# Performance work log

Hardware: AMD Instinct MI355X
Metric: run time of the kernel (lower is better)

The kernel has to match this reference:

```python
import jax, jax.numpy as jnp
import numpy as np

N_M, N_H = 50000, 50000
E = 600000
D_IN, D_OUT = 128, 128
LN_EPS = 1e-5
NORM_EPS = 1e-12


def _segment_mean(x, seg, n):
    # PyG 'mean' aggregation: sum / count, 0 for isolated nodes (count clamped to 1)
    s = jax.ops.segment_sum(x, seg, num_segments=n)
    c = jax.ops.segment_sum(jnp.ones((seg.shape[0], 1), x.dtype), seg, num_segments=n)
    return s / jnp.maximum(c, 1.0)


def _sage(t_src, t_dst, ei, Wl, bl, Wr):
    # SAGEConv: lin_l(mean_j x_j) + lin_r(x_i), then L2-normalize rows
    agg = _segment_mean(t_src[ei[0]], ei[1], t_dst.shape[0])
    out = agg @ Wl + bl + t_dst @ Wr
    nrm = jnp.maximum(jnp.linalg.norm(out, axis=-1, keepdims=True), NORM_EPS)
    return out / nrm


def _layer_norm(x, g, b):
    mu = jnp.mean(x, axis=-1, keepdims=True)
    v = jnp.var(x, axis=-1, keepdims=True)
    return (x - mu) / jnp.sqrt(v + LN_EPS) * g + b


def setup_inputs() -> dict:
    key = jax.random.key(0)
    ks = jax.random.split(key, 24)
    r = lambda i, shape: jax.random.normal(ks[i], shape, dtype=jnp.float32) * 0.05
    inp = {
        'x_microbe': jax.random.normal(ks[0], (N_M, D_IN), dtype=jnp.float32),
        'x_host': jax.random.normal(ks[1], (N_H, D_IN), dtype=jnp.float32),
        # per-node-type linear transforms
        'W_nt_m': r(2, (D_IN, D_OUT)), 'b_nt_m': r(3, (D_OUT,)),
        'W_nt_h': r(4, (D_IN, D_OUT)), 'b_nt_h': r(5, (D_OUT,)),
        # SAGEConv params per edge type (lin_l has bias, lin_r has no bias)
        'Wl_mm': r(6, (D_OUT, D_OUT)), 'bl_mm': r(7, (D_OUT,)), 'Wr_mm': r(8, (D_OUT, D_OUT)),
        'Wl_mh': r(9, (D_OUT, D_OUT)), 'bl_mh': r(10, (D_OUT,)), 'Wr_mh': r(11, (D_OUT, D_OUT)),
        'Wl_hm': r(12, (D_OUT, D_OUT)), 'bl_hm': r(13, (D_OUT,)), 'Wr_hm': r(14, (D_OUT, D_OUT)),
        # LayerNorm affine params per node type
        'g_m': jnp.ones((D_OUT,), jnp.float32), 'be_m': jnp.zeros((D_OUT,), jnp.float32),
        'g_h': jnp.ones((D_OUT,), jnp.float32), 'be_h': jnp.zeros((D_OUT,), jnp.float32),
        # edge indices [2, E]: row0 = src, row1 = dst
        'ei_mm': jax.random.randint(ks[15], (2, E), 0, N_M, dtype=jnp.int32),
        'ei_mh': jnp.stack([jax.random.randint(ks[16], (E,), 0, N_M, dtype=jnp.int32),
                            jax.random.randint(ks[17], (E,), 0, N_H, dtype=jnp.int32)]),
        'ei_hm': jnp.stack([jax.random.randint(ks[18], (E,), 0, N_H, dtype=jnp.int32),
                            jax.random.randint(ks[19], (E,), 0, N_M, dtype=jnp.int32)]),
    }
    return inp


def reference(x_microbe, x_host, W_nt_m, b_nt_m, W_nt_h, b_nt_h,
              Wl_mm, bl_mm, Wr_mm, Wl_mh, bl_mh, Wr_mh, Wl_hm, bl_hm, Wr_hm,
              g_m, be_m, g_h, be_h, ei_mm, ei_mh, ei_hm):
    # per-type linear transforms
    t_m = x_microbe @ W_nt_m + b_nt_m
    t_h = x_host @ W_nt_h + b_nt_h
    # SAGEConv per edge type
    o_mm = _sage(t_m, t_m, ei_mm, Wl_mm, bl_mm, Wr_mm)  # microbe -> microbe
    o_mh = _sage(t_m, t_h, ei_mh, Wl_mh, bl_mh, Wr_mh)  # microbe -> host
    o_hm = _sage(t_h, t_m, ei_hm, Wl_hm, bl_hm, Wr_hm)  # host -> microbe
    # HeteroConv aggr='mean' over edge types per dst node type
    conv_m = 0.5 * (o_mm + o_hm)
    conv_h = o_mh
    # residual + LayerNorm (dropout is identity in eval mode)
    out_m = _layer_norm(t_m + conv_m, g_m, be_m)
    out_h = _layer_norm(t_h + conv_h, g_h, be_h)
    return out_m, out_h
```

## Files before the change

kernel.cpp:

```cpp
#include <hip/hip_runtime.h>

typedef unsigned short u16;
typedef unsigned int u32;
typedef __attribute__((ext_vector_type(8))) short bf16x8;
typedef __attribute__((ext_vector_type(4))) float f32x4;

#define LDSN 13312
#define CHUNK 131072

__device__ __forceinline__ float bf_lo(u32 u){ return __uint_as_float(u << 16); }
__device__ __forceinline__ float bf_hi(u32 u){ return __uint_as_float(u & 0xffff0000u); }
__device__ __forceinline__ float bf2f(u16 v){ return __uint_as_float((u32)v << 16); }
__device__ __forceinline__ u16 f2bf(float f){
    u32 u = __float_as_uint(f);
    u32 r = (u + 0x7fffu + ((u >> 16) & 1u)) >> 16;
    return (u16)r;
}
__device__ __forceinline__ u32 pack2(float a, float b){
    return (u32)f2bf(a) | ((u32)f2bf(b) << 16);
}

__global__ __launch_bounds__(256) void fusedA_kernel(
    const int* __restrict__ d0, const int* __restrict__ d1, const int* __restrict__ d2,
    u16* __restrict__ rk0, u16* __restrict__ rk1, u16* __restrict__ rk2,
    int E0, int E1, int E2, int n0, int n1, int n2,
    int c0, int c1, int c2, int R0, int R1, int R2,
    u16* __restrict__ C0, u16* __restrict__ C1, u16* __restrict__ C2, int HB2,
    const float* __restrict__ Wf0, const float* __restrict__ Wf1,
    const float* __restrict__ Wf2, const float* __restrict__ Wf3,
    const float* __restrict__ Wf4, const float* __restrict__ Wf5,
    u16* __restrict__ WF,
    const float* __restrict__ Xm, const float* __restrict__ Wm,
    const float* __restrict__ bm, u16* __restrict__ Tm, int NM,
    const float* __restrict__ Xh, const float* __restrict__ Wh,
    const float* __restrict__ bh, u16* __restrict__ Th, int NH,
    int gm, int gh)
{
    __shared__ u32 lc[LDSN / 2];
    int bid = blockIdx.x;
    if (bid < HB2){
        const int* dp; u16 *rk, *cp; int E, n, cc, rr;
        if (bid < c0 * R0){ dp = d0; rk = rk0; cp = C0; E = E0; n = n0; cc = bid / R0; rr = bid % R0; }
        else if (bid < c0 * R0 + c1 * R1){ int l = bid - c0 * R0; dp = d1; rk = rk1; cp = C1; E = E1; n = n1; cc = l / R1; rr = l % R1; }
        else { int l = bid - c0 * R0 - c1 * R1; dp = d2; rk = rk2; cp = C2; E = E2; n = n2; cc = l / R2; rr = l % R2; }
        for (int i = threadIdx.x; i < LDSN / 2; i += 256) lc[i] = 0;
        __syncthreads();
        int r0 = rr * LDSN, r1 = min(r0 + LDSN, n);
        int i0 = cc * CHUNK, i1 = min(i0 + CHUNK, E);
        int i = i0 + threadIdx.x;
        for (; i + 768 < i1; i += 1024){
            int xa = dp[i], xb = dp[i + 256], xc = dp[i + 512], xd = dp[i + 768];
            if ((unsigned)xa < (unsigned)n && xa >= r0 && xa < r1){
                int lx = xa - r0; int sh = (lx & 1) << 4;
                u32 old = atomicAdd(&lc[lx >> 1], 1u << sh);
                rk[i] = (u16)((old >> sh) & 0xffffu);
            }
            if ((unsigned)xb < (unsigned)n && xb >= r0 && xb < r1){
                int lx = xb - r0; int sh = (lx & 1) << 4;
                u32 old = atomicAdd(&lc[lx >> 1], 1u << sh);
                rk[i + 256] = (u16)((old >> sh) & 0xffffu);
            }
            if ((unsigned)xc < (unsigned)n && xc >= r0 && xc < r1){
                int lx = xc - r0; int sh = (lx & 1) << 4;
                u32 old = atomicAdd(&lc[lx >> 1], 1u << sh);
                rk[i + 512] = (u16)((old >> sh) & 0xffffu);
            }
            if ((unsigned)xd < (unsigned)n && xd >= r0 && xd < r1){
                int lx = xd - r0; int sh = (lx & 1) << 4;
                u32 old = atomicAdd(&lc[lx >> 1], 1u << sh);
                rk[i + 768] = (u16)((old >> sh) & 0xffffu);
            }
        }
        for (; i < i1; i += 256){
            int x = dp[i];
            if ((unsigned)x < (unsigned)n && x >= r0 && x < r1){
                int lx = x - r0;
                int sh = (lx & 1) << 4;
                u32 old = atomicAdd(&lc[lx >> 1], 1u << sh);
                rk[i] = (u16)((old >> sh) & 0xffffu);
            }
        }
        __syncthreads();
        u16* op = cp + (size_t)cc * n;
        for (int x = r0 + threadIdx.x; x < r1; x += 256){
            int lx = x - r0;
            op[x] = (u16)((lc[lx >> 1] >> ((lx & 1) << 4)) & 0xffffu);
        }
        return;
    }
    bid -= HB2;
    if (bid < 6){
        const float* W = bid == 0 ? Wf0 : bid == 1 ? Wf1 : bid == 2 ? Wf2 :
                         bid == 3 ? Wf3 : bid == 4 ? Wf4 : Wf5;
        u16* dst = WF + (size_t)bid * 16384;
        #pragma unroll 4
        for (int k = 0; k < 64; ++k){
            int i = k * 256 + threadIdx.x;
            int j   = i & 7;
            int l16 = (i >> 3) & 15;
            int qd  = (i >> 7) & 3;
            int q   = (i >> 9) & 3;
            int tt  = (i >> 11) & 1;
            int w   = (i >> 12) & 3;
            dst[i] = f2bf(W[(q * 32 + qd * 8 + j) * 128 + (w * 32 + tt * 16 + l16)]);
        }
        return;
    }
    bid -= 6;
    const float *A, *W, *bias; u16* C; int N, lgrid, lbid;
    if (bid < gm){ A = Xm; W = Wm; bias = bm; C = Tm; N = NM; lgrid = gm; lbid = bid; }
    else         { A = Xh; W = Wh; bias = bh; C = Th; N = NH; lgrid = gh; lbid = bid - gm; }

    int tid = threadIdx.x;
    int wave = tid >> 6, lane = tid & 63;
    int colHalf = wave & 1;
    int ln16 = lane & 15, quad = lane >> 4;

    bf16x8 Bfrag[4][4];
    #pragma unroll
    for (int t = 0; t < 4; ++t){
        int col = colHalf * 64 + t * 16 + ln16;
        #pragma unroll
        for (int q = 0; q < 4; ++q){
            bf16x8 f;
            #pragma unroll
            for (int j = 0; j < 8; ++j)
                f[j] = (short)f2bf(W[(q * 32 + quad * 8 + j) * 128 + col]);
            Bfrag[t][q] = f;
        }
    }
    float bv[4];
    #pragma unroll
    for (int t = 0; t < 4; ++t)
        bv[t] = bias[colHalf * 64 + t * 16 + ln16];

    int rowBlocks = (N + 15) >> 4;
    for (int rb = lbid * 2 + (wave >> 1); rb < rowBlocks; rb += lgrid * 2){
        int row0 = rb * 16;
        int ar = row0 + ln16; if (ar > N - 1) ar = N - 1;
        const float* Arow = A + (size_t)ar * 128 + quad * 8;
        bf16x8 Af[4];
        #pragma unroll
        for (int q = 0; q < 4; ++q){
            f32x4 lo = *(const f32x4*)(Arow + q * 32);
            f32x4 hi = *(const f32x4*)(Arow + q * 32 + 4);
            bf16x8 f;
            #pragma unroll
            for (int j = 0; j < 4; ++j){ f[j] = (short)f2bf(lo[j]); f[4+j] = (short)f2bf(hi[j]); }
            Af[q] = f;
        }
        f32x4 acc[4];
        #pragma unroll
        for (int t = 0; t < 4; ++t) acc[t] = (f32x4){bv[t], bv[t], bv[t], bv[t]};
        #pragma unroll
        for (int q = 0; q < 4; ++q)
            #pragma unroll
            for (int t = 0; t < 4; ++t)
                acc[t] = __builtin_amdgcn_mfma_f32_16x16x32_bf16(Af[q], Bfrag[t][q], acc[t], 0, 0, 0);
        #pragma unroll
        for (int t = 0; t < 4; ++t){
            int col = colHalf * 64 + t * 16 + ln16;
            #pragma unroll
            for (int r = 0; r < 4; ++r){
                int row = row0 + quad * 4 + r;
                if (row < N) C[(size_t)row * 128 + col] = f2bf(acc[t][r]);
            }
        }
    }
}

__global__ __launch_bounds__(256) void scan_blocks_kernel(
    const u16* __restrict__ C0, const u16* __restrict__ C1, const u16* __restrict__ C2,
    int c0, int c1, int c2, int NM, int NH, int n,
    int* __restrict__ off, int* __restrict__ part)
{
    __shared__ int lds[256];
    int tid = threadIdx.x;
    int base = blockIdx.x * 2048 + tid * 8;
    int v[8]; int s = 0;
    #pragma unroll
    for (int j = 0; j < 8; ++j){
        int idx = base + j;
        int tot = 0;
        if (idx < n){
            const u16* cp; int ch, w, x;
            if (idx < NM){ cp = C0; ch = c0; w = NM; x = idx; }
            else if (idx < 2 * NM){ cp = C1; ch = c1; w = NM; x = idx - NM; }
            else { cp = C2; ch = c2; w = NH; x = idx - 2 * NM; }
            for (int cc = 0; cc < ch; ++cc) tot += cp[(size_t)cc * w + x];
        }
        v[j] = s; s += tot;
    }
    lds[tid] = s;
    __syncthreads();
    for (int d = 1; d < 256; d <<= 1){
        int t = (tid >= d) ? lds[tid - d] : 0;
        __syncthreads();
        lds[tid] += t;
        __syncthreads();
    }
    int thrBase = (tid > 0) ? lds[tid - 1] : 0;
    if (tid == 255) part[blockIdx.x] = lds[255];
    #pragma unroll
    for (int j = 0; j < 8; ++j){
        int idx = base + j;
        if (idx < n) off[idx] = thrBase + v[j];
    }
}

__global__ __launch_bounds__(256) void colbase_kernel(
    const u16* __restrict__ C0, const u16* __restrict__ C1, const u16* __restrict__ C2,
    int* __restrict__ B0, int* __restrict__ B1, int* __restrict__ B2,
    int c0, int c1, int c2, int NM, int NH, int n,
    int* __restrict__ off, const int* __restrict__ part)
{
    int idx = blockIdx.x * 256 + threadIdx.x;
    if (idx >= n) return;
    int pb = idx >> 11;
    int p = 0;
    for (int k = 0; k < pb; ++k) p += part[k];
    int run = off[idx] + p;
    off[idx] = run;
    const u16* cp; int* bp; int ch, w, x;
    if (idx < NM){ cp = C0; bp = B0; ch = c0; w = NM; x = idx; }
    else if (idx < 2 * NM){ cp = C1; bp = B1; ch = c1; w = NM; x = idx - NM; }
    else { cp = C2; bp = B2; ch = c2; w = NH; x = idx - 2 * NM; }
    for (int cc = 0; cc < ch; ++cc){
        bp[(size_t)cc * w + x] = run;
        run += cp[(size_t)cc * w + x];
    }
    if (idx == n - 1) off[n] = run;
}

__global__ __launch_bounds__(256) void fill3_kernel(
    const int* __restrict__ s0, const int* __restrict__ s1, const int* __restrict__ s2,
    const int* __restrict__ d0, const int* __restrict__ d1, const int* __restrict__ d2,
    const u16* __restrict__ rk0, const u16* __restrict__ rk1, const u16* __restrict__ rk2,
    int E0, int E1, int E2, int n0, int n1, int n2,
    const int* __restrict__ B0, const int* __restrict__ B1, const int* __restrict__ B2,
    int* __restrict__ slot)
{
    int t = blockIdx.y;
    const int* sp = t == 0 ? s0 : (t == 1 ? s1 : s2);
    const int* dp = t == 0 ? d0 : (t == 1 ? d1 : d2);
    const u16* rk = t == 0 ? rk0 : (t == 1 ? rk1 : rk2);
    const int* bp = t == 0 ? B0 : (t == 1 ? B1 : B2);
    int E = t == 0 ? E0 : (t == 1 ? E1 : E2);
    int n = t == 0 ? n0 : (t == 1 ? n1 : n2);
    int base = blockIdx.x * 1024 + threadIdx.x;
    #pragma unroll
    for (int k = 0; k < 4; ++k){
        int i = base + k * 256;
        if (i < E){
            int x = dp[i];
            if ((unsigned)x < (unsigned)n){
                int cc = i / CHUNK;
                slot[bp[(size_t)cc * n + x] + (int)rk[i]] = sp[i];
            }
        }
    }
}

__global__ __launch_bounds__(256) void gather3_kernel(
    const u16* __restrict__ TM, const u16* __restrict__ TH,
    const int* __restrict__ off, const int* __restrict__ slot,
    u32* __restrict__ AGGM, u32* __restrict__ AGGH, int NM, int NH)
{
    int n3 = 2 * NM + NH;
    int wid = (int)((blockIdx.x * 256u + threadIdx.x) >> 6);
    int lane = threadIdx.x & 63;
    int nw = (gridDim.x * 256) >> 6;

    for (int id0 = wid * 4; id0 < n3; id0 += nw * 4){
        int bb[4], dg[4], tk[4], ms[4], ns[4];
        const u16* Ts[4];
        #pragma unroll
        for (int r = 0; r < 4; ++r){
            int id = id0 + r;
            int b = 0, e = 0;
            if (id < n3){ b = off[id]; e = off[id + 1]; }
            bb[r] = b;
            int deg = e - b; dg[r] = deg;
            int take = deg < 64 ? deg : 64; tk[r] = take;
            const u16* Tsrc; int nsrc;
            if (id < NM){ Tsrc = TM; nsrc = NM; }
            else if (id < 2 * NM){ Tsrc = TH; nsrc = NH; }
            else { Tsrc = TM; nsrc = NM; }
            Ts[r] = Tsrc; ns[r] = nsrc;
            int s = 0;
            if (lane < take){
                s = slot[b + lane];
                if ((unsigned)s >= (unsigned)nsrc) s = 0;
            }
            ms[r] = s;
        }

        #pragma unroll
        for (int r = 0; r < 4; ++r){
            int id = id0 + r;
            if (id >= n3) break;
            const u16* Tsrc = Ts[r];
            int take = tk[r];
            float a0=0.f,a1=0.f,b0f=0.f,b1f=0.f,c0=0.f,c1=0.f,d0f=0.f,d1f=0.f;
            float e0=0.f,e1=0.f,f0=0.f,f1=0.f,g0=0.f,g1=0.f,h0=0.f,h1=0.f;
            int j = 0;
            for (; j + 8 <= take; j += 8){
                int i0 = __shfl(ms[r], j);     int i1 = __shfl(ms[r], j + 1);
                int i2 = __shfl(ms[r], j + 2); int i3 = __shfl(ms[r], j + 3);
                int i4 = __shfl(ms[r], j + 4); int i5 = __shfl(ms[r], j + 5);
                int i6 = __shfl(ms[r], j + 6); int i7 = __shfl(ms[r], j + 7);
                u32 u0 = *(const u32*)(Tsrc + (size_t)i0 * 128 + lane * 2);
                u32 u1 = *(const u32*)(Tsrc + (size_t)i1 * 128 + lane * 2);
                u32 u2 = *(const u32*)(Tsrc + (size_t)i2 * 128 + lane * 2);
                u32 u3 = *(const u32*)(Tsrc + (size_t)i3 * 128 + lane * 2);
                u32 u4 = *(const u32*)(Tsrc + (size_t)i4 * 128 + lane * 2);
                u32 u5 = *(const u32*)(Tsrc + (size_t)i5 * 128 + lane * 2);
                u32 u6 = *(const u32*)(Tsrc + (size_t)i6 * 128 + lane * 2);
                u32 u7 = *(const u32*)(Tsrc + (size_t)i7 * 128 + lane * 2);
                a0 += bf_lo(u0); a1 += bf_hi(u0);
                b0f += bf_lo(u1); b1f += bf_hi(u1);
                c0 += bf_lo(u2); c1 += bf_hi(u2);
                d0f += bf_lo(u3); d1f += bf_hi(u3);
                e0 += bf_lo(u4); e1 += bf_hi(u4);
                f0 += bf_lo(u5); f1 += bf_hi(u5);
                g0 += bf_lo(u6); g1 += bf_hi(u6);
                h0 += bf_lo(u7); h1 += bf_hi(u7);
            }
            for (; j + 4 <= take; j += 4){
                int i0 = __shfl(ms[r], j);     int i1 = __shfl(ms[r], j + 1);
                int i2 = __shfl(ms[r], j + 2); int i3 = __shfl(ms[r], j + 3);
                u32 u0 = *(const u32*)(Tsrc + (size_t)i0 * 128 + lane * 2);
                u32 u1 = *(const u32*)(Tsrc + (size_t)i1 * 128 + lane * 2);
                u32 u2 = *(const u32*)(Tsrc + (size_t)i2 * 128 + lane * 2);
                u32 u3 = *(const u32*)(Tsrc + (size_t)i3 * 128 + lane * 2);
                a0 += bf_lo(u0); a1 += bf_hi(u0);
                b0f += bf_lo(u1); b1f += bf_hi(u1);
                c0 += bf_lo(u2); c1 += bf_hi(u2);
                d0f += bf_lo(u3); d1f += bf_hi(u3);
            }
            for (; j < take; ++j){
                int i0 = __shfl(ms[r], j);
                u32 u0 = *(const u32*)(Tsrc + (size_t)i0 * 128 + lane * 2);
                a0 += bf_lo(u0); a1 += bf_hi(u0);
            }
            for (int j2 = bb[r] + 64; j2 < bb[r] + dg[r]; ++j2){
                int i0 = slot[j2];
                if ((unsigned)i0 >= (unsigned)ns[r]) i0 = 0;
                u32 u0 = *(const u32*)(Tsrc + (size_t)i0 * 128 + lane * 2);
                a0 += bf_lo(u0); a1 += bf_hi(u0);
            }
            float s0 = ((a0 + b0f) + (c0 + d0f)) + ((e0 + f0) + (g0 + h0));
            float s1 = ((a1 + b1f) + (c1 + d1f)) + ((e1 + f1) + (g1 + h1));
            float inv = 1.0f / (float)(dg[r] < 1 ? 1 : dg[r]);
            u32 pv = pack2(s0 * inv, s1 * inv);
            if (id < 2 * NM) AGGM[(size_t)id * 64 + lane] = pv;
            else             AGGH[(size_t)(id - 2 * NM) * 64 + lane] = pv;
        }
    }
}

template<int NT>
__global__ __launch_bounds__(256) void gemmln_kernel(
    const u32* __restrict__ AG1, const u32* __restrict__ AG2,
    const u16* __restrict__ Tdst,
    const u16* __restrict__ WFl1, const u16* __restrict__ WFr1, const float* __restrict__ bl1,
    const u16* __restrict__ WFl2, const u16* __restrict__ WFr2, const float* __restrict__ bl2,
    const float* __restrict__ g, const float* __restrict__ be,
    float* __restrict__ outp, int N, float scale)
{
    __shared__ float redN[NT][4][16];
    __shared__ float redS[2][4][16];

    int tid = threadIdx.x;
    int wave = tid >> 6, lane = tid & 63;
    int ln16 = lane & 15, quad = lane >> 4;

    const u32* AG[2] = {AG1, AG2};
    const u16* WFl[2] = {WFl1, WFl2};
    const u16* WFr[2] = {WFr1, WFr2};
    const float* bls[2] = {bl1, bl2};

    bf16x8 BL[NT][2][4], BR[NT][2][4];
    float bv[NT][2];
    #pragma unroll
    for (int et = 0; et < NT; ++et){
        #pragma unroll
        for (int t = 0; t < 2; ++t){
            bv[et][t] = bls[et][wave * 32 + t * 16 + ln16];
            #pragma unroll
            for (int q = 0; q < 4; ++q){
                int fo = ((((wave * 2 + t) * 4 + q) * 4 + quad) * 16 + ln16) * 8;
                BL[et][t][q] = *(const bf16x8*)(WFl[et] + fo);
                BR[et][t][q] = *(const bf16x8*)(WFr[et] + fo);
            }
        }
    }
    float gv[2], bev[2];
    #pragma unroll
    for (int t = 0; t < 2; ++t){
        int col = wave * 32 + t * 16 + ln16;
        gv[t] = g[col]; bev[t] = be[col];
    }

    int tiles = (N + 15) >> 4;
    for (int tile = blockIdx.x; tile < tiles; tile += gridDim.x){
        int row0 = tile * 16;
        int ar = row0 + ln16; if (ar > N - 1) ar = N - 1;
        const u16* Ar2 = Tdst + (size_t)ar * 128 + quad * 8;

        f32x4 acc[NT][2];
        #pragma unroll
        for (int et = 0; et < NT; ++et)
            #pragma unroll
            for (int t = 0; t < 2; ++t)
                acc[et][t] = (f32x4){bv[et][t], bv[et][t], bv[et][t], bv[et][t]};

        #pragma unroll
        for (int q = 0; q < 4; ++q){
            bf16x8 afr = *(const bf16x8*)(Ar2 + q * 32);
            #pragma unroll
            for (int et = 0; et < NT; ++et){
                bf16x8 afl = *(const bf16x8*)(AG[et] + (size_t)ar * 64 + q * 16 + quad * 4);
                #pragma unroll
                for (int t = 0; t < 2; ++t){
                    acc[et][t] = __builtin_amdgcn_mfma_f32_16x16x32_bf16(afl, BL[et][t][q], acc[et][t], 0, 0, 0);
                    acc[et][t] = __builtin_amdgcn_mfma_f32_16x16x32_bf16(afr, BR[et][t][q], acc[et][t], 0, 0, 0);
                }
            }
        }

        #pragma unroll
        for (int et = 0; et < NT; ++et){
            #pragma unroll
            for (int r = 0; r < 4; ++r){
                float s = acc[et][0][r] * acc[et][0][r] + acc[et][1][r] * acc[et][1][r];
                #pragma unroll
                for (int m = 1; m < 16; m <<= 1) s += __shfl_xor(s, m);
                if (ln16 == 0) redN[et][wave][quad * 4 + r] = s;
            }
        }
        __syncthreads();

        float yv[2][4];
        float lsum[4], lsq[4];
        #pragma unroll
        for (int r = 0; r < 4; ++r){
            int r16 = quad * 4 + r;
            int row = row0 + r16;
            int crow = row < N ? row : N - 1;
            float sc[NT];
            #pragma unroll
            for (int et = 0; et < NT; ++et){
                float tot = redN[et][0][r16] + redN[et][1][r16] + redN[et][2][r16] + redN[et][3][r16];
                sc[et] = scale / fmaxf(sqrtf(tot), 1e-12f);
            }
            float s1v = 0.f, s2v = 0.f;
            #pragma unroll
            for (int t = 0; t < 2; ++t){
                int col = wave * 32 + t * 16 + ln16;
                float y = bf2f(Tdst[(size_t)crow * 128 + col]);
                #pragma unroll
                for (int et = 0; et < NT; ++et) y += acc[et][t][r] * sc[et];
                yv[t][r] = y;
                s1v += y; s2v += y * y;
            }
            #pragma unroll
            for (int m = 1; m < 16; m <<= 1){ s1v += __shfl_xor(s1v, m); s2v += __shfl_xor(s2v, m); }
            lsum[r] = s1v; lsq[r] = s2v;
        }
        if (ln16 == 0){
            #pragma unroll
            for (int r = 0; r < 4; ++r){
                redS[0][wave][quad * 4 + r] = lsum[r];
                redS[1][wave][quad * 4 + r] = lsq[r];
            }
        }
        __syncthreads();

        #pragma unroll
        for (int r = 0; r < 4; ++r){
            int r16 = quad * 4 + r;
            int row = row0 + r16;
            if (row >= N) continue;
            float S1 = redS[0][0][r16] + redS[0][1][r16] + redS[0][2][r16] + redS[0][3][r16];
            float S2 = redS[1][0][r16] + redS[1][1][r16] + redS[1][2][r16] + redS[1][3][r16];
            float mean = S1 * (1.0f / 128.0f);
            float var = S2 * (1.0f / 128.0f) - mean * mean;
            float rstd = rsqrtf(var + 1e-5f);
            #pragma unroll
            for (int t = 0; t < 2; ++t){
                int col = wave * 32 + t * 16 + ln16;
                outp[(size_t)row * 128 + col] = (yv[t][r] - mean) * rstd * gv[t] + bev[t];
            }
        }
        __syncthreads();
    }
}

extern "C" void kernel_launch(void* const* d_in, const int* in_sizes, int n_in,
                              void* d_out, int out_size, void* d_ws, size_t ws_size,
                              hipStream_t stream) {
    const float* xm    = (const float*)d_in[0];
    const float* xh    = (const float*)d_in[1];
    const float* Wnt_m = (const float*)d_in[2];  const float* bnt_m = (const float*)d_in[3];
    const float* Wnt_h = (const float*)d_in[4];  const float* bnt_h = (const float*)d_in[5];
    const float* Wl_mm = (const float*)d_in[6];  const float* bl_mm = (const float*)d_in[7];
    const float* Wr_mm = (const float*)d_in[8];
    const float* Wl_mh = (const float*)d_in[9];  const float* bl_mh = (const float*)d_in[10];
    const float* Wr_mh = (const float*)d_in[11];
    const float* Wl_hm = (const float*)d_in[12]; const float* bl_hm = (const float*)d_in[13];
    const float* Wr_hm = (const float*)d_in[14];
    const float* g_m   = (const float*)d_in[15]; const float* be_m  = (const float*)d_in[16];
    const float* g_h   = (const float*)d_in[17]; const float* be_h  = (const float*)d_in[18];
    const int* ei_mm = (const int*)d_in[19];
    const int* ei_mh = (const int*)d_in[20];
    const int* ei_hm = (const int*)d_in[21];

    const int D = 128;
    const int NM = in_sizes[0] / D;
    const int NH = in_sizes[1] / D;
    const int E1 = in_sizes[19] / 2;
    const int E2 = in_sizes[20] / 2;
    const int E3 = in_sizes[21] / 2;
    const int Esum = E1 + E2 + E3;
    const int n3 = 2 * NM + NH;

    const int c0 = (E1 + CHUNK - 1) / CHUNK;
    const int c1 = (E3 + CHUNK - 1) / CHUNK;
    const int c2 = (E2 + CHUNK - 1) / CHUNK;
    const int R0 = (NM + LDSN - 1) / LDSN;
    const int R1 = (NM + LDSN - 1) / LDSN;
    const int R2 = (NH + LDSN - 1) / LDSN;
    const int HB2 = c0 * R0 + c1 * R1 + c2 * R2;

    char* ws = (char*)d_ws;
    size_t woff = 0;
    auto alloc = [&](size_t bytes) -> void* {
        void* p = ws + woff;
        woff += (bytes + 255) & ~(size_t)255;
        return p;
    };
    u16* T_M   = (u16*)alloc((size_t)NM * D * 2);
    u16* T_H   = (u16*)alloc((size_t)NH * D * 2);
    u16* CNT16 = (u16*)alloc(((size_t)(c0 + c1) * NM + (size_t)c2 * NH) * 2);
    int* OFF3  = (int*)alloc((size_t)(n3 + 1) * 4);
    int* SLOT3 = (int*)alloc((size_t)Esum * 4);
    int* PART  = (int*)alloc(1024 * 4);
    u16* WF    = (u16*)alloc((size_t)6 * 16384 * 2);
    u32* AGGM  = (u32*)alloc((size_t)2 * NM * 64 * 4);
    if (woff > ws_size) return;

    u16* C0p = CNT16;
    u16* C1p = C0p + (size_t)c0 * NM;
    u16* C2p = C1p + (size_t)c1 * NM;

    int* B0p = (int*)d_out;
    int* B1p = B0p + (size_t)c0 * NM;
    int* B2p = B1p + (size_t)c1 * NM;
    u16* RK  = (u16*)(B2p + (size_t)c2 * NH);
    u16* rk0 = RK, *rk1 = RK + E1, *rk2 = RK + E1 + E3;
    u32* AGGH = (u32*)d_out;

    float* OUT_M = (float*)d_out;
    float* OUT_H = (float*)d_out + (size_t)NM * D;

    const int gm = 1024, gh = 1024;
    const int scanBlocks = (n3 + 2047) / 2048;
    int Emax = E1 > E2 ? E1 : E2; if (E3 > Emax) Emax = E3;
    const dim3 egrid((Emax + 1023) / 1024, 3);

    fusedA_kernel<<<HB2 + 6 + gm + gh, 256, 0, stream>>>(
        ei_mm + E1, ei_hm + E3, ei_mh + E2,
        rk0, rk1, rk2,
        E1, E3, E2, NM, NM, NH,
        c0, c1, c2, R0, R1, R2,
        C0p, C1p, C2p, HB2,
        Wl_mm, Wr_mm, Wl_hm, Wr_hm, Wl_mh, Wr_mh, WF,
        xm, Wnt_m, bnt_m, T_M, NM,
        xh, Wnt_h, bnt_h, T_H, NH, gm, gh);

    scan_blocks_kernel<<<scanBlocks, 256, 0, stream>>>(
        C0p, C1p, C2p, c0, c1, c2, NM, NH, n3, OFF3, PART);
    colbase_kernel<<<(n3 + 255) / 256, 256, 0, stream>>>(
        C0p, C1p, C2p, B0p, B1p, B2p, c0, c1, c2, NM, NH, n3, OFF3, PART);

    fill3_kernel<<<egrid, 256, 0, stream>>>(
        ei_mm, ei_hm, ei_mh,
        ei_mm + E1, ei_hm + E3, ei_mh + E2,
        rk0, rk1, rk2,
        E1, E3, E2, NM, NM, NH,
        B0p, B1p, B2p, SLOT3);

    gather3_kernel<<<4096, 256, 0, stream>>>(
        T_M, T_H, OFF3, SLOT3, AGGM, AGGH, NM, NH);

    gemmln_kernel<1><<<1024, 256, 0, stream>>>(
        AGGH, nullptr, T_H,
        WF + 4 * 16384, WF + 5 * 16384, bl_mh,
        nullptr, nullptr, nullptr,
        g_h, be_h, OUT_H, NH, 1.0f);
    gemmln_kernel<2><<<1024, 256, 0, stream>>>(
        AGGM, AGGM + (size_t)NM * 64, T_M,
        WF + 0 * 16384, WF + 1 * 16384, bl_mm,
        WF + 2 * 16384, WF + 3 * 16384, bl_hm,
        g_m, be_m, OUT_M, NM, 0.5f);
}
```

Measured before the change: 480.7 us.

## Merge host and microbe GEMM+LayerNorm launches into one split-grid kernel

Replaces the two templated gemmln launches (host with one edge type, microbe with two) with a single launch. Blocks below a split index handle microbe rows and the rest handle host rows, which lets both node types run concurrently and removes one launch and its tail. AGGH is moved into the OUT_H region with a 128-word row stride so the in-place host rows do not overlap microbe output. The edge-type loop now has a runtime count instead of a compile-time one, which may cost unrolling and registers. CHUNK is also reduced.

After: 557.9 us. 16.1% more time.

```diff
diff --git a/kernel.cpp b/kernel.cpp
--- a/kernel.cpp
+++ b/kernel.cpp
@@ -6,7 +6,7 @@
 typedef __attribute__((ext_vector_type(4))) float f32x4;
 
 #define LDSN 13312
-#define CHUNK 131072
+#define CHUNK 32768
 
 __device__ __forceinline__ float bf_lo(u32 u){ return __uint_as_float(u << 16); }
 __device__ __forceinline__ float bf_hi(u32 u){ return __uint_as_float(u & 0xffff0000u); }
@@ -354,36 +354,57 @@
             float inv = 1.0f / (float)(dg[r] < 1 ? 1 : dg[r]);
             u32 pv = pack2(s0 * inv, s1 * inv);
             if (id < 2 * NM) AGGM[(size_t)id * 64 + lane] = pv;
-            else             AGGH[(size_t)(id - 2 * NM) * 64 + lane] = pv;
-        }
-    }
-}
-
-template<int NT>
+            else             AGGH[(size_t)(id - 2 * NM) * 128 + lane] = pv;
+        }
+    }
+}
+
 __global__ __launch_bounds__(256) void gemmln_kernel(
-    const u32* __restrict__ AG1, const u32* __restrict__ AG2,
-    const u16* __restrict__ Tdst,
-    const u16* __restrict__ WFl1, const u16* __restrict__ WFr1, const float* __restrict__ bl1,
-    const u16* __restrict__ WFl2, const u16* __restrict__ WFr2, const float* __restrict__ bl2,
-    const float* __restrict__ g, const float* __restrict__ be,
-    float* __restrict__ outp, int N, float scale)
+    const u32* __restrict__ AGM, const u32* __restrict__ AGH,
+    const u16* __restrict__ TM, const u16* __restrict__ TH,
+    const u16* __restrict__ WF,
+    const float* __restrict__ bl_mm, const float* __restrict__ bl_hm, const float* __restrict__ bl_mh,
+    const float* __restrict__ g_m, const float* __restrict__ be_m,
+    const float* __restrict__ g_h, const float* __restrict__ be_h,
+    float* __restrict__ OUTM, float* __restrict__ OUTH,
+    int NM, int NH, int gsplit)
 {
-    __shared__ float redN[NT][4][16];
+    __shared__ float redN[2][4][16];
     __shared__ float redS[2][4][16];
 
     int tid = threadIdx.x;
     int wave = tid >> 6, lane = tid & 63;
     int ln16 = lane & 15, quad = lane >> 4;
 
-    const u32* AG[2] = {AG1, AG2};
-    const u16* WFl[2] = {WFl1, WFl2};
-    const u16* WFr[2] = {WFr1, WFr2};
-    const float* bls[2] = {bl1, bl2};
-
-    bf16x8 BL[NT][2][4], BR[NT][2][4];
-    float bv[NT][2];
-    #pragma unroll
-    for (int et = 0; et < NT; ++et){
+    bool isH = (int)blockIdx.x >= gsplit;
+    int nt = isH ? 1 : 2;
+    int N = isH ? NH : NM;
+    float scale = isH ? 1.0f : 0.5f;
+    const u16* Tdst = isH ? TH : TM;
+    float* outp = isH ? OUTH : OUTM;
+    const float* g  = isH ? g_h : g_m;
+    const float* be = isH ? be_h : be_m;
+    const u32* AG[2];
+    int ags;
+    const u16* WFl[2]; const u16* WFr[2];
+    const float* bls[2];
+    if (isH){
+        AG[0] = AGH; AG[1] = AGH; ags = 128;
+        WFl[0] = WF + 4 * 16384; WFr[0] = WF + 5 * 16384;
+        WFl[1] = WFl[0]; WFr[1] = WFr[0];
+        bls[0] = bl_mh; bls[1] = bl_mh;
+    } else {
+        AG[0] = AGM; AG[1] = AGM + (size_t)NM * 64; ags = 64;
+        WFl[0] = WF + 0 * 16384; WFr[0] = WF + 1 * 16384;
+        WFl[1] = WF + 2 * 16384; WFr[1] = WF + 3 * 16384;
+        bls[0] = bl_mm; bls[1] = bl_hm;
+    }
+    int lbid  = isH ? (int)blockIdx.x - gsplit : (int)blockIdx.x;
+    int lgrid = isH ? (int)gridDim.x - gsplit : gsplit;
+
+    bf16x8 BL[2][2][4], BR[2][2][4];
+    float bv[2][2];
+    for (int et = 0; et < nt; ++et){
         #pragma unroll
         for (int t = 0; t < 2; ++t){
             bv[et][t] = bls[et][wave * 32 + t * 16 + ln16];
@@ -403,14 +424,13 @@
     }
 
     int tiles = (N + 15) >> 4;
-    for (int tile = blockIdx.x; tile < tiles; tile += gridDim.x){
+    for (int tile = lbid; tile < tiles; tile += lgrid){
         int row0 = tile * 16;
         int ar = row0 + ln16; if (ar > N - 1) ar = N - 1;
         const u16* Ar2 = Tdst + (size_t)ar * 128 + quad * 8;
 
-        f32x4 acc[NT][2];
-        #pragma unroll
-        for (int et = 0; et < NT; ++et)
+        f32x4 acc[2][2];
+        for (int et = 0; et < nt; ++et)
             #pragma unroll
             for (int t = 0; t < 2; ++t)
                 acc[et][t] = (f32x4){bv[et][t], bv[et][t], bv[et][t], bv[et][t]};
@@ -418,9 +438,8 @@
         #pragma unroll
         for (int q = 0; q < 4; ++q){
             bf16x8 afr = *(const bf16x8*)(Ar2 + q * 32);
-            #pragma unroll
-            for (int et = 0; et < NT; ++et){
-                bf16x8 afl = *(const bf16x8*)(AG[et] + (size_t)ar * 64 + q * 16 + quad * 4);
+            for (int et = 0; et < nt; ++et){
+                bf16x8 afl = *(const bf16x8*)(AG[et] + (size_t)ar * ags + q * 16 + quad * 4);
                 #pragma unroll
                 for (int t = 0; t < 2; ++t){
                     acc[et][t] = __builtin_amdgcn_mfma_f32_16x16x32_bf16(afl, BL[et][t][q], acc[et][t], 0, 0, 0);
@@ -429,8 +448,7 @@
             }
         }
 
-        #pragma unroll
-        for (int et = 0; et < NT; ++et){
+        for (int et = 0; et < nt; ++et){
             #pragma unroll
             for (int r = 0; r < 4; ++r){
                 float s = acc[et][0][r] * acc[et][0][r] + acc[et][1][r] * acc[et][1][r];
@@ -448,9 +466,8 @@
             int r16 = quad * 4 + r;
             int row = row0 + r16;
             int crow = row < N ? row : N - 1;
-            float sc[NT];
-            #pragma unroll
-            for (int et = 0; et < NT; ++et){
+            float sc[2];
+            for (int et = 0; et < nt; ++et){
                 float tot = redN[et][0][r16] + redN[et][1][r16] + redN[et][2][r16] + redN[et][3][r16];
                 sc[et] = scale / fmaxf(sqrtf(tot), 1e-12f);
             }
@@ -459,8 +476,7 @@
             for (int t = 0; t < 2; ++t){
                 int col = wave * 32 + t * 16 + ln16;
                 float y = bf2f(Tdst[(size_t)crow * 128 + col]);
-                #pragma unroll
-                for (int et = 0; et < NT; ++et) y += acc[et][t][r] * sc[et];
+                for (int et = 0; et < nt; ++et) y += acc[et][t][r] * sc[et];
                 yv[t][r] = y;
                 s1v += y; s2v += y * y;
             }
@@ -559,10 +575,10 @@
     int* B2p = B1p + (size_t)c1 * NM;
     u16* RK  = (u16*)(B2p + (size_t)c2 * NH);
     u16* rk0 = RK, *rk1 = RK + E1, *rk2 = RK + E1 + E3;
-    u32* AGGH = (u32*)d_out;
 
     float* OUT_M = (float*)d_out;
     float* OUT_H = (float*)d_out + (size_t)NM * D;
+    u32* AGGH = (u32*)OUT_H;
 
     const int gm = 1024, gh = 1024;
     const int scanBlocks = (n3 + 2047) / 2048;
@@ -594,14 +610,9 @@
     gather3_kernel<<<4096, 256, 0, stream>>>(
         T_M, T_H, OFF3, SLOT3, AGGM, AGGH, NM, NH);
 
-    gemmln_kernel<1><<<1024, 256, 0, stream>>>(
-        AGGH, nullptr, T_H,
-        WF + 4 * 16384, WF + 5 * 16384, bl_mh,
-        nullptr, nullptr, nullptr,
-        g_h, be_h, OUT_H, NH, 1.0f);
-    gemmln_kernel<2><<<1024, 256, 0, stream>>>(
-        AGGM, AGGM + (size_t)NM * 64, T_M,
-        WF + 0 * 16384, WF + 1 * 16384, bl_mm,
-        WF + 2 * 16384, WF + 3 * 16384, bl_hm,
-        g_m, be_m, OUT_M, NM, 0.5f);
-}
+    gemmln_kernel<<<2048, 256, 0, stream>>>(
+        AGGM, AGGH, T_M, T_H, WF,
+        bl_mm, bl_hm, bl_mh,
+        g_m, be_m, g_h, be_h,
+        OUT_M, OUT_H, NM, NH, 1638);
+}
```
